# Optimization experiments

Hardware: AMD Instinct MI355X
Metric: run time of the kernel (lower is better)

Reference implementation:

```python
import jax, jax.numpy as jnp
import numpy as np

BN_EPS = 1e-5

def _gin_conv(h, src, dst, W, b, n_nodes):
    # GINConv with eps=0: MLP(x + sum_{j->i} x_j)
    agg = jax.ops.segment_sum(h[src], dst, num_segments=n_nodes)  # [N,H]
    z = h + agg
    z = jax.nn.relu(z @ W[0] + b[0])
    z = jax.nn.relu(z @ W[1] + b[1])
    z = z @ W[2] + b[2]
    return z

def _batch_norm(z, gamma, beta):
    # training-mode BatchNorm1d over the node (batch) dimension
    mean = jnp.mean(z, axis=0)
    var = jnp.var(z, axis=0)
    return (z - mean) * jax.lax.rsqrt(var + BN_EPS) * gamma + beta

def setup_inputs() -> dict:
    key = jax.random.key(0)
    ks = jax.random.split(key, 8)
    N, E, IN, H, OUT = 50000, 800000, 128, 128, 64
    x = jax.random.normal(ks[0], (N, IN), dtype=jnp.float32)
    edge_index = jax.random.randint(ks[1], (2, E), 0, N, dtype=jnp.int64)
    convW = jax.random.normal(ks[2], (3, 3, H, H), dtype=jnp.float32) * 0.05
    convB = jnp.zeros((3, 3, H), dtype=jnp.float32)
    bn_gamma = jnp.ones((3, H), dtype=jnp.float32)
    bn_beta = jnp.zeros((3, H), dtype=jnp.float32)
    linW = jax.random.normal(ks[3], (3 * H, H), dtype=jnp.float32) * 0.05
    linB = jnp.zeros((H,), dtype=jnp.float32)
    clsW = jax.random.normal(ks[4], (H, OUT), dtype=jnp.float32) * 0.05
    clsB = jnp.zeros((OUT,), dtype=jnp.float32)
    return {"x": x, "edge_index": edge_index, "convW": convW, "convB": convB,
            "bn_gamma": bn_gamma, "bn_beta": bn_beta, "linW": linW, "linB": linB,
            "clsW": clsW, "clsB": clsB}

def reference(x, edge_index, convW, convB, bn_gamma, bn_beta, linW, linB, clsW, clsB):
    N = x.shape[0]
    src, dst = edge_index[0], edge_index[1]
    h1 = jax.nn.relu(_batch_norm(_gin_conv(x, src, dst, convW[0], convB[0], N), bn_gamma[0], bn_beta[0]))
    h2 = jax.nn.relu(_batch_norm(_gin_conv(h1, src, dst, convW[1], convB[1], N), bn_gamma[1], bn_beta[1]))
    h3 = _batch_norm(_gin_conv(h2, src, dst, convW[2], convB[2], N), bn_gamma[2], bn_beta[2])
    h = jnp.concatenate([h1, h2, h3], axis=1) @ linW + linB  # [N,H]
    # dropout p=0.5 treated as identity (eval mode)
    logits = h @ clsW + clsB  # [N,OUT]
    return (logits, h)
```

## Files before the change

### kernel.cpp

```cpp
#include <hip/hip_runtime.h>
#include <hip/hip_bf16.h>
#include <stdint.h>


using bf16x8 = __attribute__((ext_vector_type(8))) short;
using f32x4  = __attribute__((ext_vector_type(4))) float;

__device__ inline short f2bf(float f) {
    union { __hip_bfloat16 h; short s; } u;
    u.h = __float2bfloat16(f);
    return u.s;
}
__device__ inline float bf2f(short s) {
    union { uint32_t u; float f; } c;
    c.u = ((uint32_t)(uint16_t)s) << 16;
    return c.f;
}


__global__ void zero_int_k(int* __restrict__ p, int n) {
    int i = blockIdx.x * blockDim.x + threadIdx.x;
    if (i < n) p[i] = 0;
}

__global__ void deg_count_k(const int* __restrict__ dst, int* __restrict__ deg, int E) {
    int e = blockIdx.x * blockDim.x + threadIdx.x;
    if (e < E) atomicAdd(&deg[dst[e]], 1);
}

__global__ __launch_bounds__(512) void chunk_reduce_k(const int* __restrict__ deg,
                                                      int* __restrict__ chunkSum, int N) {
    __shared__ int s[512];
    int i = blockIdx.x * 512 + threadIdx.x;
    s[threadIdx.x] = (i < N) ? deg[i] : 0;
    __syncthreads();
    for (int off = 256; off > 0; off >>= 1) {
        if (threadIdx.x < off) s[threadIdx.x] += s[threadIdx.x + off];
        __syncthreads();
    }
    if (threadIdx.x == 0) chunkSum[blockIdx.x] = s[0];
}

__global__ void scan_chunks_k(int* __restrict__ chunkSum, int* __restrict__ rowPtr,
                              int nchunks, int N) {
    if (threadIdx.x == 0 && blockIdx.x == 0) {
        int run = 0;
        for (int b = 0; b < nchunks; b++) {
            int v = chunkSum[b];
            chunkSum[b] = run;
            run += v;
        }
        rowPtr[N] = run;
    }
}

__global__ __launch_bounds__(512) void expand_scan_k(const int* __restrict__ deg,
                                                     const int* __restrict__ chunkOff,
                                                     int* __restrict__ rowPtr,
                                                     int* __restrict__ cursor, int N) {
    __shared__ int s[512];
    const int t = threadIdx.x;
    const int i = blockIdx.x * 512 + t;
    const int v = (i < N) ? deg[i] : 0;
    s[t] = v;
    __syncthreads();
    for (int off = 1; off < 512; off <<= 1) {
        int u = (t >= off) ? s[t - off] : 0;
        __syncthreads();
        s[t] += u;
        __syncthreads();
    }
    if (i < N) {
        int excl = s[t] - v + chunkOff[blockIdx.x];
        rowPtr[i] = excl;
        cursor[i] = excl;
    }
}

__global__ void fill_k(const int* __restrict__ src, const int* __restrict__ dst,
                       int* __restrict__ cursor, int* __restrict__ sortedSrc, int E) {
    int e = blockIdx.x * blockDim.x + threadIdx.x;
    if (e < E) {
        int pos = atomicAdd(&cursor[dst[e]], 1);
        sortedSrc[pos] = src[e];
    }
}

__global__ __launch_bounds__(256) void transpose_w_k(const float* __restrict__ convW,
                                                     const float* __restrict__ linW,
                                                     const float* __restrict__ clsW,
                                                     short* __restrict__ Wt) {
    const int b = blockIdx.x;
    const float* src;
    int NC;
    if (b < 9)       { src = convW + (size_t)b * 16384;      NC = 128; }
    else if (b < 12) { src = linW + (size_t)(b - 9) * 16384; NC = 128; }
    else             { src = clsW;                            NC = 64; }
    short* dst = Wt + (size_t)b * 16384;
    const int tot = NC * 32;
    for (int i = threadIdx.x; i < tot; i += 256) {
        int n = i >> 5, k0 = (i & 31) << 2;
        short4 s;
        s.x = f2bf(src[(k0 + 0) * NC + n]);
        s.y = f2bf(src[(k0 + 1) * NC + n]);
        s.z = f2bf(src[(k0 + 2) * NC + n]);
        s.w = f2bf(src[(k0 + 3) * NC + n]);
        *(short4*)&dst[n * 128 + k0] = s;
    }
}

__global__ void cast16_k(const float* __restrict__ x, short* __restrict__ x16, int n4) {
    int i = blockIdx.x * blockDim.x + threadIdx.x;
    int stride = gridDim.x * blockDim.x;
    for (; i < n4; i += stride) {
        float4 v = ((const float4*)x)[i];
        short4 s = {f2bf(v.x), f2bf(v.y), f2bf(v.z), f2bf(v.w)};
        ((short4*)x16)[i] = s;
    }
}

__global__ void zero_f_k(float* __restrict__ p, int n) {
    int i = blockIdx.x * blockDim.x + threadIdx.x;
    if (i < n) p[i] = 0.f;
}

__global__ void bnparam_k(const float* __restrict__ stats, const float* __restrict__ gamma,
                          const float* __restrict__ beta, float* __restrict__ sb, int N) {
    int c = threadIdx.x;
    float inv = 1.f / (float)N;
    float mean = stats[c] * inv;
    float var = stats[128 + c] * inv - mean * mean;
    float s = gamma[c] * rsqrtf(var + 1e-5f);
    sb[c] = s;
    sb[128 + c] = beta[c] - mean * s;
}

template <bool AFFINE>
__global__ __launch_bounds__(256) void agg16_k(const short* __restrict__ h16,
                                               const int* __restrict__ sortedSrc,
                                               const int* __restrict__ rowPtr,
                                               const float* __restrict__ sb,
                                               short* __restrict__ B16, int N) {
    const int node = blockIdx.x * 8 + (threadIdx.x >> 5);
    if (node >= N) return;
    const int f4 = (threadIdx.x & 31) << 2;
    float s0 = 1.f, s1 = 1.f, s2 = 1.f, s3 = 1.f, t0 = 0.f, t1 = 0.f, t2 = 0.f, t3 = 0.f;
    if (AFFINE) {
        float4 sv = *(const float4*)&sb[f4];
        float4 tv = *(const float4*)&sb[128 + f4];
        s0 = sv.x; s1 = sv.y; s2 = sv.z; s3 = sv.w;
        t0 = tv.x; t1 = tv.y; t2 = tv.z; t3 = tv.w;
    }
    float a0 = 0.f, a1 = 0.f, a2 = 0.f, a3 = 0.f;

#define GACC(v) { \
    float x0 = bf2f((v).x), x1 = bf2f((v).y), x2 = bf2f((v).z), x3 = bf2f((v).w); \
    if (AFFINE) { \
        x0 = fmaxf(fmaf(x0, s0, t0), 0.f); x1 = fmaxf(fmaf(x1, s1, t1), 0.f); \
        x2 = fmaxf(fmaf(x2, s2, t2), 0.f); x3 = fmaxf(fmaf(x3, s3, t3), 0.f); } \
    a0 += x0; a1 += x1; a2 += x2; a3 += x3; }

    short4 self = *(const short4*)&h16[(size_t)node * 128 + f4];
    GACC(self);

    const int beg = rowPtr[node], end = rowPtr[node + 1];
    int j = beg;
    for (; j + 4 <= end; j += 4) {
        int i0 = sortedSrc[j], i1 = sortedSrc[j + 1], i2 = sortedSrc[j + 2], i3 = sortedSrc[j + 3];
        short4 v0 = *(const short4*)&h16[(size_t)i0 * 128 + f4];
        short4 v1 = *(const short4*)&h16[(size_t)i1 * 128 + f4];
        short4 v2 = *(const short4*)&h16[(size_t)i2 * 128 + f4];
        short4 v3 = *(const short4*)&h16[(size_t)i3 * 128 + f4];
        GACC(v0); GACC(v1); GACC(v2); GACC(v3);
    }
    for (; j < end; j++) {
        int ii = sortedSrc[j];
        short4 v = *(const short4*)&h16[(size_t)ii * 128 + f4];
        GACC(v);
    }
#undef GACC

    short4 o = {f2bf(a0), f2bf(a1), f2bf(a2), f2bf(a3)};
    *(short4*)&B16[(size_t)node * 128 + f4] = o;
}

__global__ __launch_bounds__(256) void mlp_layer_k(const short* __restrict__ B16,
                                                   const short* __restrict__ Wt0,
                                                   const short* __restrict__ Wt1,
                                                   const short* __restrict__ Wt2,
                                                   const float* __restrict__ b0,
                                                   const float* __restrict__ b1,
                                                   const float* __restrict__ b2,
                                                   short* __restrict__ Z16,
                                                   float* __restrict__ stats, int N) {
    constexpr int LR = 136;
    __shared__ __align__(16) short sA[64 * LR];
    __shared__ __align__(16) short sW[128 * LR];
    __shared__ float sStats[256];
    const int t = threadIdx.x;
    const int row0 = blockIdx.x * 64;
    const int w = t >> 6, l = t & 63;
    const int lr = l & 15, lg = l >> 4;

    sStats[t] = 0.f;
    for (int i = t; i < 64 * 16; i += 256) {
        int r = i >> 4, k0 = (i & 15) << 3;
        int gr = row0 + r;
        bf16x8 v = {0, 0, 0, 0, 0, 0, 0, 0};
        if (gr < N) v = *(const bf16x8*)&B16[(size_t)gr * 128 + k0];
        *(bf16x8*)&sA[r * LR + k0] = v;
    }

    const short* Ws[3] = {Wt0, Wt1, Wt2};
    const float* bs[3] = {b0, b1, b2};

    for (int ph = 0; ph < 3; ph++) {
        __syncthreads();
        for (int i = t; i < 128 * 16; i += 256) {
            int n = i >> 4, k0 = (i & 15) << 3;
            *(bf16x8*)&sW[n * LR + k0] = *(const bf16x8*)&Ws[ph][n * 128 + k0];
        }
        __syncthreads();

        bf16x8 af[4];
#pragma unroll
        for (int kb = 0; kb < 4; kb++)
            af[kb] = *(const bf16x8*)&sA[(w * 16 + lr) * LR + kb * 32 + lg * 8];

        f32x4 acc[8];
#pragma unroll
        for (int n = 0; n < 8; n++) acc[n] = {0.f, 0.f, 0.f, 0.f};
#pragma unroll
        for (int n = 0; n < 8; n++)
#pragma unroll
            for (int kb = 0; kb < 4; kb++) {
                bf16x8 bf = *(const bf16x8*)&sW[(n * 16 + lr) * LR + kb * 32 + lg * 8];
                acc[n] = __builtin_amdgcn_mfma_f32_16x16x32_bf16(af[kb], bf, acc[n], 0, 0, 0);
            }

        const float* bias = bs[ph];
        if (ph < 2) {
#pragma unroll
            for (int n = 0; n < 8; n++) {
                const int col = n * 16 + lr;
                const float bv = bias[col];
#pragma unroll
                for (int j = 0; j < 4; j++) {
                    int rloc = w * 16 + lg * 4 + j;
                    float v = fmaxf(acc[n][j] + bv, 0.f);
                    sA[rloc * LR + col] = f2bf(v);
                }
            }
        } else {
#pragma unroll
            for (int n = 0; n < 8; n++) {
                const int col = n * 16 + lr;
                const float bv = bias[col];
                float part = 0.f, part2 = 0.f;
#pragma unroll
                for (int j = 0; j < 4; j++) {
                    int r = row0 + w * 16 + lg * 4 + j;
                    if (r < N) {
                        float v = acc[n][j] + bv;
                        Z16[(size_t)r * 128 + col] = f2bf(v);
                        part += v; part2 += v * v;
                    }
                }
                atomicAdd(&sStats[col], part);
                atomicAdd(&sStats[128 + col], part2);
            }
        }
    }
    __syncthreads();
    atomicAdd(&stats[t], sStats[t]);
}

__global__ __launch_bounds__(256) void fuse3_k(const short* __restrict__ Z0,
                                               const short* __restrict__ Z1,
                                               const short* __restrict__ Z2,
                                               const float* __restrict__ sb,
                                               const short* __restrict__ Wt,
                                               const float* __restrict__ linB,
                                               const float* __restrict__ clsB,
                                               float* __restrict__ hout,
                                               float* __restrict__ logits, int N) {
    constexpr int LR = 136;
    __shared__ __align__(16) short sA[64 * LR];
    __shared__ __align__(16) short sW[128 * LR];
    __shared__ __align__(16) short sH[64 * LR];
    const int t = threadIdx.x;
    const int row0 = blockIdx.x * 64;
    const int w = t >> 6, l = t & 63;
    const int lr = l & 15, lg = l >> 4;

    const short* Zs[3] = {Z0, Z1, Z2};

    f32x4 acc[8];
#pragma unroll
    for (int n = 0; n < 8; n++) acc[n] = {0.f, 0.f, 0.f, 0.f};

    for (int s = 0; s < 3; s++) {
        const short* Zsrc = Zs[s];
        const short* Wsrc = Wt + (size_t)(9 + s) * 16384;
        const float* ss = sb + (size_t)s * 256;
        const float* tt = ss + 128;
        for (int i = t; i < 128 * 16; i += 256) {
            int n = i >> 4, k0 = (i & 15) << 3;
            *(bf16x8*)&sW[n * LR + k0] = *(const bf16x8*)&Wsrc[n * 128 + k0];
        }
        for (int i = t; i < 64 * 16; i += 256) {
            int r = i >> 4, k0 = (i & 15) << 3;
            int gr = row0 + r;
            bf16x8 v = {0, 0, 0, 0, 0, 0, 0, 0};
            if (gr < N) {
                bf16x8 z = *(const bf16x8*)&Zsrc[(size_t)gr * 128 + k0];
#pragma unroll
                for (int e = 0; e < 8; e++) {
                    float xv = fmaf(bf2f(z[e]), ss[k0 + e], tt[k0 + e]);
                    if (s < 2) xv = fmaxf(xv, 0.f);
                    v[e] = f2bf(xv);
                }
            }
            *(bf16x8*)&sA[r * LR + k0] = v;
        }
        __syncthreads();
        bf16x8 af[4];
#pragma unroll
        for (int kb = 0; kb < 4; kb++)
            af[kb] = *(const bf16x8*)&sA[(w * 16 + lr) * LR + kb * 32 + lg * 8];
#pragma unroll
        for (int n = 0; n < 8; n++)
#pragma unroll
            for (int kb = 0; kb < 4; kb++) {
                bf16x8 bf = *(const bf16x8*)&sW[(n * 16 + lr) * LR + kb * 32 + lg * 8];
                acc[n] = __builtin_amdgcn_mfma_f32_16x16x32_bf16(af[kb], bf, acc[n], 0, 0, 0);
            }
        __syncthreads();
    }

#pragma unroll
    for (int n = 0; n < 8; n++) {
        const int col = n * 16 + lr;
        const float bv = linB[col];
#pragma unroll
        for (int j = 0; j < 4; j++) {
            int rloc = w * 16 + lg * 4 + j;
            int r = row0 + rloc;
            float v = acc[n][j] + bv;
            if (r < N) hout[(size_t)r * 128 + col] = v;
            sH[rloc * LR + col] = f2bf(v);
        }
    }
    for (int i = t; i < 64 * 16; i += 256) {
        int n = i >> 4, k0 = (i & 15) << 3;
        *(bf16x8*)&sW[n * LR + k0] = *(const bf16x8*)&Wt[(size_t)12 * 16384 + n * 128 + k0];
    }
    __syncthreads();

    bf16x8 ah[4];
#pragma unroll
    for (int kb = 0; kb < 4; kb++)
        ah[kb] = *(const bf16x8*)&sH[(w * 16 + lr) * LR + kb * 32 + lg * 8];

    f32x4 acc2[4];
#pragma unroll
    for (int n = 0; n < 4; n++) acc2[n] = {0.f, 0.f, 0.f, 0.f};
#pragma unroll
    for (int n = 0; n < 4; n++)
#pragma unroll
        for (int kb = 0; kb < 4; kb++) {
            bf16x8 bf = *(const bf16x8*)&sW[(n * 16 + lr) * LR + kb * 32 + lg * 8];
            acc2[n] = __builtin_amdgcn_mfma_f32_16x16x32_bf16(ah[kb], bf, acc2[n], 0, 0, 0);
        }
#pragma unroll
    for (int n = 0; n < 4; n++) {
        const int col = n * 16 + lr;
        const float bv = clsB[col];
#pragma unroll
        for (int j = 0; j < 4; j++) {
            int r = row0 + w * 16 + lg * 4 + j;
            if (r < N) logits[(size_t)r * 64 + col] = acc2[n][j] + bv;
        }
    }
}


extern "C" void kernel_launch(void* const* d_in, const int* in_sizes, int n_in,
                              void* d_out, int out_size, void* d_ws, size_t ws_size,
                              hipStream_t stream) {
    const float* x     = (const float*)d_in[0];
    const int*   ei    = (const int*)d_in[1];
    const float* convW = (const float*)d_in[2];
    const float* convB = (const float*)d_in[3];
    const float* gamma = (const float*)d_in[4];
    const float* beta  = (const float*)d_in[5];
    const float* linW  = (const float*)d_in[6];
    const float* linB  = (const float*)d_in[7];
    const float* clsW  = (const float*)d_in[8];
    const float* clsB  = (const float*)d_in[9];

    const int N = in_sizes[0] / 128;
    const int E = in_sizes[1] / 2;
    const int* src = ei;
    const int* dst = ei + E;

    short* x16 = (short*)d_ws;
    short* B16 = x16 + (size_t)N * 128;
    short* Z16 = B16 + (size_t)N * 128;
    float* stats = (float*)(Z16 + (size_t)3 * N * 128);
    float* sb    = stats + 768;
    int* deg       = (int*)(sb + 768);
    int* rowPtr    = deg + N;
    int* cursor    = rowPtr + (N + 1);
    int* chunkSum  = cursor + N;
    int* sortedSrc = chunkSum + 512;
    short* Wt = (short*)((((uintptr_t)(sortedSrc + E)) + 15) & ~(uintptr_t)15);

    float* logits = (float*)d_out;
    float* hout   = (float*)d_out + (size_t)N * 64;

    const int nchunks = (N + 511) / 512;
    const int eb = (E + 255) / 256;

    zero_int_k<<<(N + 255) / 256, 256, 0, stream>>>(deg, N);
    deg_count_k<<<eb, 256, 0, stream>>>(dst, deg, E);
    chunk_reduce_k<<<nchunks, 512, 0, stream>>>(deg, chunkSum, N);
    scan_chunks_k<<<1, 64, 0, stream>>>(chunkSum, rowPtr, nchunks, N);
    expand_scan_k<<<nchunks, 512, 0, stream>>>(deg, chunkSum, rowPtr, cursor, N);
    fill_k<<<eb, 256, 0, stream>>>(src, dst, cursor, sortedSrc, E);

    transpose_w_k<<<13, 256, 0, stream>>>(convW, linW, clsW, Wt);
    cast16_k<<<1024, 256, 0, stream>>>(x, x16, N * 32);
    zero_f_k<<<3, 256, 0, stream>>>(stats, 768);

    const int nbm = (N + 63) / 64;
    const int aggb = (N + 7) / 8;

    for (int li = 0; li < 3; li++) {
        const short* hin16 = (li == 0) ? x16 : (Z16 + (size_t)(li - 1) * N * 128);
        const float* sbl   = sb + (size_t)(li - 1) * 256;
        if (li == 0)
            agg16_k<false><<<aggb, 256, 0, stream>>>(hin16, sortedSrc, rowPtr, nullptr, B16, N);
        else
            agg16_k<true><<<aggb, 256, 0, stream>>>(hin16, sortedSrc, rowPtr, sbl, B16, N);

        const short* Wt0 = Wt + (size_t)(li * 3 + 0) * 16384;
        const short* Wt1 = Wt + (size_t)(li * 3 + 1) * 16384;
        const short* Wt2 = Wt + (size_t)(li * 3 + 2) * 16384;
        const float* b0 = convB + ((size_t)li * 3 + 0) * 128;
        const float* b1 = convB + ((size_t)li * 3 + 1) * 128;
        const float* b2 = convB + ((size_t)li * 3 + 2) * 128;
        float* statL = stats + (size_t)li * 256;

        mlp_layer_k<<<nbm, 256, 0, stream>>>(B16, Wt0, Wt1, Wt2, b0, b1, b2,
                                             Z16 + (size_t)li * N * 128, statL, N);
        bnparam_k<<<1, 128, 0, stream>>>(statL, gamma + li * 128, beta + li * 128,
                                         sb + (size_t)li * 256, N);
    }

    fuse3_k<<<nbm, 256, 0, stream>>>(Z16, Z16 + (size_t)N * 128, Z16 + (size_t)2 * N * 128,
                                     sb, Wt, linB, clsB, hout, logits, N);
}
```

Measured before the change: 490.4 us.

## Prefetch next MLP weights into registers, use per-block stat partials, unroll gather by 8

```diff
diff --git a/kernel.cpp b/kernel.cpp
--- a/kernel.cpp
+++ b/kernel.cpp
@@ -124,6 +124,17 @@
     if (i < n) p[i] = 0.f;
 }
 
+__global__ __launch_bounds__(256) void stats_reduce_k(const float* __restrict__ partial,
+                                                      float* __restrict__ stats, int nb) {
+    const int c = threadIdx.x;
+    const int b0 = blockIdx.x * 16;
+    const int bend = min(nb, b0 + 16);
+    float s = 0.f;
+    for (int b = b0; b < bend; b++)
+        s += partial[(size_t)b * 256 + c];
+    atomicAdd(&stats[c], s);
+}
+
 __global__ void bnparam_k(const float* __restrict__ stats, const float* __restrict__ gamma,
                           const float* __restrict__ beta, float* __restrict__ sb, int N) {
     int c = threadIdx.x;
@@ -165,6 +176,22 @@
 
     const int beg = rowPtr[node], end = rowPtr[node + 1];
     int j = beg;
+    for (; j + 8 <= end; j += 8) {
+        int i0 = sortedSrc[j + 0], i1 = sortedSrc[j + 1];
+        int i2 = sortedSrc[j + 2], i3 = sortedSrc[j + 3];
+        int i4 = sortedSrc[j + 4], i5 = sortedSrc[j + 5];
+        int i6 = sortedSrc[j + 6], i7 = sortedSrc[j + 7];
+        short4 v0 = *(const short4*)&h16[(size_t)i0 * 128 + f4];
+        short4 v1 = *(const short4*)&h16[(size_t)i1 * 128 + f4];
+        short4 v2 = *(const short4*)&h16[(size_t)i2 * 128 + f4];
+        short4 v3 = *(const short4*)&h16[(size_t)i3 * 128 + f4];
+        short4 v4 = *(const short4*)&h16[(size_t)i4 * 128 + f4];
+        short4 v5 = *(const short4*)&h16[(size_t)i5 * 128 + f4];
+        short4 v6 = *(const short4*)&h16[(size_t)i6 * 128 + f4];
+        short4 v7 = *(const short4*)&h16[(size_t)i7 * 128 + f4];
+        GACC(v0); GACC(v1); GACC(v2); GACC(v3);
+        GACC(v4); GACC(v5); GACC(v6); GACC(v7);
+    }
     for (; j + 4 <= end; j += 4) {
         int i0 = sortedSrc[j], i1 = sortedSrc[j + 1], i2 = sortedSrc[j + 2], i3 = sortedSrc[j + 3];
         short4 v0 = *(const short4*)&h16[(size_t)i0 * 128 + f4];
@@ -192,7 +219,7 @@
                                                    const float* __restrict__ b1,
                                                    const float* __restrict__ b2,
                                                    short* __restrict__ Z16,
-                                                   float* __restrict__ stats, int N) {
+                                                   float* __restrict__ partial, int N) {
     constexpr int LR = 136;
     __shared__ __align__(16) short sA[64 * LR];
     __shared__ __align__(16) short sW[128 * LR];
@@ -210,17 +237,26 @@
         if (gr < N) v = *(const bf16x8*)&B16[(size_t)gr * 128 + k0];
         *(bf16x8*)&sA[r * LR + k0] = v;
     }
-
-    const short* Ws[3] = {Wt0, Wt1, Wt2};
+    for (int i = t; i < 128 * 16; i += 256) {
+        int n = i >> 4, k0 = (i & 15) << 3;
+        *(bf16x8*)&sW[n * LR + k0] = *(const bf16x8*)&Wt0[n * 128 + k0];
+    }
+
+    const short* Wnext[2] = {Wt1, Wt2};
     const float* bs[3] = {b0, b1, b2};
+    bf16x8 wpre[8];
 
     for (int ph = 0; ph < 3; ph++) {
         __syncthreads();
-        for (int i = t; i < 128 * 16; i += 256) {
-            int n = i >> 4, k0 = (i & 15) << 3;
-            *(bf16x8*)&sW[n * LR + k0] = *(const bf16x8*)&Ws[ph][n * 128 + k0];
-        }
-        __syncthreads();
+        if (ph < 2) {
+            const short* Wn = Wnext[ph];
+#pragma unroll
+            for (int q = 0; q < 8; q++) {
+                int i = t + q * 256;
+                int n = i >> 4, k0 = (i & 15) << 3;
+                wpre[q] = *(const bf16x8*)&Wn[n * 128 + k0];
+            }
+        }
 
         bf16x8 af[4];
 #pragma unroll
@@ -270,9 +306,18 @@
                 atomicAdd(&sStats[128 + col], part2);
             }
         }
+        __syncthreads();
+        if (ph < 2) {
+#pragma unroll
+            for (int q = 0; q < 8; q++) {
+                int i = t + q * 256;
+                int n = i >> 4, k0 = (i & 15) << 3;
+                *(bf16x8*)&sW[n * LR + k0] = wpre[q];
+            }
+        }
     }
     __syncthreads();
-    atomicAdd(&stats[t], sStats[t]);
+    partial[(size_t)blockIdx.x * 256 + t] = sStats[t];
 }
 
 __global__ __launch_bounds__(256) void fuse3_k(const short* __restrict__ Z0,
@@ -404,12 +449,15 @@
     const int* src = ei;
     const int* dst = ei + E;
 
+    const int nbm = (N + 63) / 64;
+
     short* x16 = (short*)d_ws;
     short* B16 = x16 + (size_t)N * 128;
     short* Z16 = B16 + (size_t)N * 128;
     float* stats = (float*)(Z16 + (size_t)3 * N * 128);
     float* sb    = stats + 768;
-    int* deg       = (int*)(sb + 768);
+    float* partial = sb + 768;
+    int* deg       = (int*)(partial + (size_t)nbm * 256);
     int* rowPtr    = deg + N;
     int* cursor    = rowPtr + (N + 1);
     int* chunkSum  = cursor + N;
@@ -433,8 +481,8 @@
     cast16_k<<<1024, 256, 0, stream>>>(x, x16, N * 32);
     zero_f_k<<<3, 256, 0, stream>>>(stats, 768);
 
-    const int nbm = (N + 63) / 64;
     const int aggb = (N + 7) / 8;
+    const int rb = (nbm + 15) / 16;
 
     for (int li = 0; li < 3; li++) {
         const short* hin16 = (li == 0) ? x16 : (Z16 + (size_t)(li - 1) * N * 128);
@@ -453,7 +501,8 @@
         float* statL = stats + (size_t)li * 256;
 
         mlp_layer_k<<<nbm, 256, 0, stream>>>(B16, Wt0, Wt1, Wt2, b0, b1, b2,
-                                             Z16 + (size_t)li * N * 128, statL, N);
+                                             Z16 + (size_t)li * N * 128, partial, N);
+        stats_reduce_k<<<rb, 256, 0, stream>>>(partial, statL, nbm);
         bnparam_k<<<1, 128, 0, stream>>>(statL, gamma + li * 128, beta + li * 128,
                                          sb + (size_t)li * 256, N);
     }
```

New measurement: 481.1 us. About the same (-1.9%).
